# Kernel optimization log

Measured on AMD Instinct MI355X. Metric: run time of the kernel, lower is better.

The kernel has to match this reference:

```python
import jax, jax.numpy as jnp
import numpy as np

D1, D2, DK, NH = 1024, 1024, 1024, 1
B, S = 4, 2048


def setup_inputs() -> dict:
    key = jax.random.key(0)
    ks = jax.random.split(key, 12)
    scale1 = 1.0 / np.sqrt(D1)
    scale2 = 1.0 / np.sqrt(D2)
    scalek = 1.0 / np.sqrt(DK)
    return {
        "x": jax.random.normal(ks[0], (B, S, D1), dtype=jnp.float32),
        "y": jax.random.normal(ks[1], (B, S, D2), dtype=jnp.float32),
        "adj": jax.random.uniform(ks[2], (B, S, S), dtype=jnp.float32),
        "Wq": jax.random.uniform(ks[3], (D1, DK), jnp.float32, -scale1, scale1),
        "bq": jax.random.uniform(ks[4], (DK,), jnp.float32, -scale1, scale1),
        "Wk": jax.random.uniform(ks[5], (D2, DK), jnp.float32, -scale2, scale2),
        "bk": jax.random.uniform(ks[6], (DK,), jnp.float32, -scale2, scale2),
        "Wv": jax.random.uniform(ks[7], (D2, DK), jnp.float32, -scale2, scale2),
        "bv": jax.random.uniform(ks[8], (DK,), jnp.float32, -scale2, scale2),
        "Wo": jax.random.uniform(ks[9], (DK, D2), jnp.float32, -scalek, scalek),
        "bo": jax.random.uniform(ks[10], (D2,), jnp.float32, -scalek, scalek),
    }


def reference(x, y, adj, Wq, bq, Wk, bk, Wv, bv, Wo, bo):
    # Single-head (n_heads=1) cross-attention with additive adjacency bias.
    dk_head = DK // NH
    norm = 1.0 / np.sqrt(DK)
    Q = (x @ Wq + bq).reshape(NH, B, S, dk_head)   # [h,b,s,d]
    K = (y @ Wk + bk).reshape(NH, B, S, dk_head)
    V = (y @ Wv + bv).reshape(NH, B, S, dk_head)
    att = jnp.einsum('hbsd,hbtd->hbst', Q, K) * norm  # [h,b,s,t]
    att = jax.nn.softmax(att + adj, axis=-1)          # adj [b,s,t] broadcasts over h
    tmp = jnp.einsum('hbst,hbtd->hbsd', att, V).reshape(B, S, -1)  # [b,s,dk]
    out = (tmp @ Wo + bo).reshape(-1, S, D2)
    return out
```

## Files before the change

### kernel.cpp

```cpp
#include <hip/hip_runtime.h>
#include <stdint.h>

typedef unsigned short u16;
using bf16x8 = __attribute__((ext_vector_type(8))) short;
using f32x4  = __attribute__((ext_vector_type(4))) float;

#define NORM 0.03125f

enum { M_BF16_BIAS = 0, M_BF16T_BIAS = 1, M_EXP = 2, M_PV = 3, M_F32_BIAS = 4 };

__device__ __forceinline__ u16 f2bf(float f) {
  uint32_t u = __float_as_uint(f);
  return (u16)((u + 0x7FFFu + ((u >> 16) & 1u)) >> 16);
}

__device__ __forceinline__ void gload_lds16(const void* g, void* lds) {
  __builtin_amdgcn_global_load_lds(
      (const __attribute__((address_space(1))) uint32_t*)g,
      (__attribute__((address_space(3))) uint32_t*)lds, 16, 0, 0);
}

__global__ void k_cvt(const float* __restrict__ in, u16* __restrict__ out, int n4) {
  int i = blockIdx.x * blockDim.x + threadIdx.x;
  if (i >= n4) return;
  float4 v = ((const float4*)in)[i];
  uint32_t lo = f2bf(v.x) | ((uint32_t)f2bf(v.y) << 16);
  uint32_t hi = f2bf(v.z) | ((uint32_t)f2bf(v.w) << 16);
  ((uint2*)out)[i] = make_uint2(lo, hi);
}

__global__ void k_tc(const float* __restrict__ W0, const float* __restrict__ W1,
                     const float* __restrict__ W2, const float* __restrict__ W3,
                     u16* __restrict__ dst) {
  __shared__ float t[64][65];
  const float* W = blockIdx.z == 0 ? W0 : blockIdx.z == 1 ? W1 : blockIdx.z == 2 ? W2 : W3;
  u16* WT = dst + (size_t)blockIdx.z * (1024 * 1024);
  int c0 = blockIdx.x * 64, r0 = blockIdx.y * 64;
  int c = threadIdx.x & 63, q = threadIdx.x >> 6;
  for (int r = q; r < 64; r += 4) t[r][c] = W[(size_t)(r0 + r) * 1024 + c0 + c];
  __syncthreads();
  for (int r = q; r < 64; r += 4) WT[(size_t)(c0 + r) * 1024 + r0 + c] = f2bf(t[c][r]);
}

template <int MODE>
__global__ __launch_bounds__(256, 2) void gemm_bt(
    const u16* __restrict__ A, int lda, const u16* __restrict__ Bsrc, int ldb,
    long long bstrideB, int K, const float* __restrict__ bias,
    const float* __restrict__ adj, float* __restrict__ dpart,
    const float* __restrict__ dpart_r, void* __restrict__ Cout, int ldc) {
  __shared__ u16 As[128 * 64];
  __shared__ u16 Bs[128 * 64];

  const int tid = threadIdx.x;
  const int lane = tid & 63;
  const int wid = tid >> 6;
  const int wr = wid >> 1, wc = wid & 1;

  const int m0 = blockIdx.x * 128;
  const int n0 = blockIdx.y * 128;
  const int b = m0 >> 11;
  const u16* Bp = Bsrc + (size_t)b * bstrideB;

  f32x4 acc[4][4] = {};

  const int ric = lane >> 3;
  const int col8 = (lane & 7) * 8;

  for (int kt = 0; kt < K; kt += 64) {
#pragma unroll
    for (int c = 0; c < 4; ++c) {
      int ch = wid * 4 + c;
      int row = ch * 8 + ric;
      gload_lds16(A + (size_t)(m0 + row) * lda + kt + col8, (void*)&As[ch * 512]);
      gload_lds16(Bp + (size_t)(n0 + row) * ldb + kt + col8, (void*)&Bs[ch * 512]);
    }
    __syncthreads();
#pragma unroll
    for (int kk = 0; kk < 64; kk += 32) {
      bf16x8 af[4], bfr[4];
#pragma unroll
      for (int m = 0; m < 4; ++m)
        af[m] = *(const bf16x8*)&As[(wr * 64 + m * 16 + (lane & 15)) * 64 + kk + (lane >> 4) * 8];
#pragma unroll
      for (int n = 0; n < 4; ++n)
        bfr[n] = *(const bf16x8*)&Bs[(wc * 64 + n * 16 + (lane & 15)) * 64 + kk + (lane >> 4) * 8];
#pragma unroll
      for (int m = 0; m < 4; ++m)
#pragma unroll
        for (int n = 0; n < 4; ++n)
          acc[m][n] = __builtin_amdgcn_mfma_f32_16x16x32_bf16(af[m], bfr[n], acc[m][n], 0, 0, 0);
    }
    __syncthreads();
  }

  const int lr = lane >> 4;
  const int lc = lane & 15;

  if constexpr (MODE == M_BF16_BIAS) {
    u16* C = (u16*)Cout;
#pragma unroll
    for (int m = 0; m < 4; ++m)
#pragma unroll
      for (int n = 0; n < 4; ++n) {
        int gcol = n0 + wc * 64 + n * 16 + lc;
        float bvv = bias[gcol];
#pragma unroll
        for (int r = 0; r < 4; ++r) {
          int grow = m0 + wr * 64 + m * 16 + lr * 4 + r;
          C[(size_t)grow * ldc + gcol] = f2bf(acc[m][n][r] + bvv);
        }
      }
  } else if constexpr (MODE == M_BF16T_BIAS) {
    u16* C = (u16*)Cout;
#pragma unroll
    for (int m = 0; m < 4; ++m)
#pragma unroll
      for (int n = 0; n < 4; ++n) {
        int gcol = n0 + wc * 64 + n * 16 + lc;
        float bvv = bias[gcol];
        int grow0 = m0 + wr * 64 + m * 16 + lr * 4;
        int t0 = grow0 & 2047;
        ushort4 pk = make_ushort4(f2bf(acc[m][n][0] + bvv), f2bf(acc[m][n][1] + bvv),
                                  f2bf(acc[m][n][2] + bvv), f2bf(acc[m][n][3] + bvv));
        *(ushort4*)&C[((size_t)b * 1024 + gcol) * 2048 + t0] = pk;
      }
  } else if constexpr (MODE == M_EXP) {
    u16* C = (u16*)Cout;
    float esum[4][4] = {};
#pragma unroll
    for (int m = 0; m < 4; ++m)
#pragma unroll
      for (int n = 0; n < 4; ++n) {
        int gcol = n0 + wc * 64 + n * 16 + lc;
#pragma unroll
        for (int r = 0; r < 4; ++r) {
          int grow = m0 + wr * 64 + m * 16 + lr * 4 + r;
          float z = acc[m][n][r] * NORM + adj[(size_t)grow * 2048 + gcol];
          float e = __expf(z);
          C[(size_t)grow * 2048 + gcol] = f2bf(e);
          esum[m][r] += e;
        }
      }
    int pidx = blockIdx.y * 2 + wc;
#pragma unroll
    for (int m = 0; m < 4; ++m)
#pragma unroll
      for (int r = 0; r < 4; ++r) {
        float s = esum[m][r];
        s += __shfl_xor(s, 1);
        s += __shfl_xor(s, 2);
        s += __shfl_xor(s, 4);
        s += __shfl_xor(s, 8);
        if (lc == 0)
          dpart[(size_t)pidx * 8192 + (m0 + wr * 64 + m * 16 + lr * 4 + r)] = s;
      }
  } else if constexpr (MODE == M_PV) {
    __shared__ float dinv[128];
    if (tid < 128) {
      float s = 0.f;
      for (int t = 0; t < 32; ++t) s += dpart_r[(size_t)t * 8192 + m0 + tid];
      dinv[tid] = 1.0f / s;
    }
    __syncthreads();
    u16* C = (u16*)Cout;
#pragma unroll
    for (int m = 0; m < 4; ++m)
#pragma unroll
      for (int n = 0; n < 4; ++n) {
        int gcol = n0 + wc * 64 + n * 16 + lc;
#pragma unroll
        for (int r = 0; r < 4; ++r) {
          int lrow = wr * 64 + m * 16 + lr * 4 + r;
          C[(size_t)(m0 + lrow) * ldc + gcol] = f2bf(acc[m][n][r] * dinv[lrow]);
        }
      }
  } else {
    float* C = (float*)Cout;
#pragma unroll
    for (int m = 0; m < 4; ++m)
#pragma unroll
      for (int n = 0; n < 4; ++n) {
        int gcol = n0 + wc * 64 + n * 16 + lc;
        float bvv = bias[gcol];
#pragma unroll
        for (int r = 0; r < 4; ++r) {
          int grow = m0 + wr * 64 + m * 16 + lr * 4 + r;
          C[(size_t)grow * ldc + gcol] = acc[m][n][r] + bvv;
        }
      }
  }
}

extern "C" void kernel_launch(void* const* d_in, const int* in_sizes, int n_in,
                              void* d_out, int out_size, void* d_ws, size_t ws_size,
                              hipStream_t stream) {
  const float* x   = (const float*)d_in[0];
  const float* y   = (const float*)d_in[1];
  const float* adj = (const float*)d_in[2];
  const float* Wq  = (const float*)d_in[3];
  const float* bq  = (const float*)d_in[4];
  const float* Wk  = (const float*)d_in[5];
  const float* bk  = (const float*)d_in[6];
  const float* Wv  = (const float*)d_in[7];
  const float* bv  = (const float*)d_in[8];
  const float* Wo  = (const float*)d_in[9];
  const float* bo  = (const float*)d_in[10];
  float* out = (float*)d_out;

  char* ws = (char*)d_ws;
  if (ws_size < 143654912ULL) return;
  u16* xb = (u16*)(ws);
  u16* yb = (u16*)(ws + 16777216);
  u16* WT = (u16*)(ws + 33554432);
  u16* Qb = (u16*)(ws + 41943040);
  u16* Kb = (u16*)(ws + 58720256);
  u16* Vt = (u16*)(ws + 75497472);
  u16* E  = (u16*)(ws + 92274688);
  float* dpart = (float*)(ws + 125829120);
  u16* tmpb = (u16*)(ws + 126877696);

  u16* WqT = WT;
  u16* WkT = WT + 1048576;
  u16* WvT = WT + 2097152;
  u16* WoT = WT + 3145728;

  k_cvt<<<8192, 256, 0, stream>>>(x, xb, 2097152);
  k_cvt<<<8192, 256, 0, stream>>>(y, yb, 2097152);
  k_tc<<<dim3(16, 16, 4), 256, 0, stream>>>(Wq, Wk, Wv, Wo, WT);

  gemm_bt<M_BF16_BIAS><<<dim3(64, 8), 256, 0, stream>>>(
      xb, 1024, WqT, 1024, 0, 1024, bq, nullptr, nullptr, nullptr, Qb, 1024);
  gemm_bt<M_BF16_BIAS><<<dim3(64, 8), 256, 0, stream>>>(
      yb, 1024, WkT, 1024, 0, 1024, bk, nullptr, nullptr, nullptr, Kb, 1024);
  gemm_bt<M_BF16T_BIAS><<<dim3(64, 8), 256, 0, stream>>>(
      yb, 1024, WvT, 1024, 0, 1024, bv, nullptr, nullptr, nullptr, Vt, 2048);

  gemm_bt<M_EXP><<<dim3(64, 16), 256, 0, stream>>>(
      Qb, 1024, Kb, 1024, 2097152LL, 1024, nullptr, adj, dpart, nullptr, E, 2048);

  gemm_bt<M_PV><<<dim3(64, 8), 256, 0, stream>>>(
      E, 2048, Vt, 2048, 2097152LL, 2048, nullptr, nullptr, nullptr, dpart, tmpb, 1024);

  gemm_bt<M_F32_BIAS><<<dim3(64, 8), 256, 0, stream>>>(
      tmpb, 1024, WoT, 1024, 0, 1024, bo, nullptr, nullptr, nullptr, out, 1024);
}
```

Measured before the change: 271.5 us.

## Replace GEMMs with 256x256 double-buffered swizzled kernel and merge QKV launches

Replaces the 128x128, 4-wave GEMM with a 256x256-tile, 8-wave kernel. It double-buffers a 128 KB LDS stage, uses XOR-swizzled LDS layouts, and issues the next K-slices' async global-to-LDS loads between MFMA phases, with explicit vmcnt/lgkmcnt waits and s_setprio. The Q, K and V projections are merged into one launch indexed by blockIdx.z. The goal is more data reuse per tile and hiding load latency behind MFMA. In exchange, grids shrink, so the PV and output GEMMs launch only 128 blocks, and the large LDS footprint limits occupancy to one block per CU.

```diff
diff --git a/kernel.cpp b/kernel.cpp
--- a/kernel.cpp
+++ b/kernel.cpp
@@ -7,7 +7,7 @@
 
 #define NORM 0.03125f
 
-enum { M_BF16_BIAS = 0, M_BF16T_BIAS = 1, M_EXP = 2, M_PV = 3, M_F32_BIAS = 4 };
+enum { M_PROJ = 0, M_EXP = 1, M_PV = 2, M_OUT = 3 };
 
 __device__ __forceinline__ u16 f2bf(float f) {
   uint32_t u = __float_as_uint(f);
@@ -42,152 +42,223 @@
   for (int r = q; r < 64; r += 4) WT[(size_t)(c0 + r) * 1024 + r0 + c] = f2bf(t[c][r]);
 }
 
+struct GArgs {
+  const u16* A; const u16* B; int lda, ldb; long long bstrideB; int K;
+  const float* bias; const float* adj; float* dpart; const float* dpart_r;
+  void* C; int ldc;
+  const u16* A1; const u16* B1; const u16* B2;
+  const float* bias1; const float* bias2; void* C1; void* C2;
+};
+
 template <int MODE>
-__global__ __launch_bounds__(256, 2) void gemm_bt(
-    const u16* __restrict__ A, int lda, const u16* __restrict__ Bsrc, int ldb,
-    long long bstrideB, int K, const float* __restrict__ bias,
-    const float* __restrict__ adj, float* __restrict__ dpart,
-    const float* __restrict__ dpart_r, void* __restrict__ Cout, int ldc) {
-  __shared__ u16 As[128 * 64];
-  __shared__ u16 Bs[128 * 64];
-
-  const int tid = threadIdx.x;
-  const int lane = tid & 63;
-  const int wid = tid >> 6;
-  const int wr = wid >> 1, wc = wid & 1;
-
-  const int m0 = blockIdx.x * 128;
-  const int n0 = blockIdx.y * 128;
+__global__ __launch_bounds__(512, 2) void gemm8(GArgs g) {
+  __shared__ __align__(16) u16 sm[65536];
+
+  const int tid = threadIdx.x, lane = tid & 63, wid = tid >> 6;
+  const int wm = wid >> 2, wn = wid & 3;
+  const int m0 = blockIdx.x * 256;
+  const int n0 = blockIdx.y * 256;
   const int b = m0 >> 11;
-  const u16* Bp = Bsrc + (size_t)b * bstrideB;
-
-  f32x4 acc[4][4] = {};
-
-  const int ric = lane >> 3;
-  const int col8 = (lane & 7) * 8;
-
-  for (int kt = 0; kt < K; kt += 64) {
-#pragma unroll
-    for (int c = 0; c < 4; ++c) {
-      int ch = wid * 4 + c;
-      int row = ch * 8 + ric;
-      gload_lds16(A + (size_t)(m0 + row) * lda + kt + col8, (void*)&As[ch * 512]);
-      gload_lds16(Bp + (size_t)(n0 + row) * ldb + kt + col8, (void*)&Bs[ch * 512]);
+
+  const u16* A = g.A; const u16* B = g.B;
+  const float* bias = g.bias; void* C = g.C;
+  int zmode = 0;
+  if constexpr (MODE == M_PROJ) {
+    int z = blockIdx.z; zmode = z;
+    if (z == 1) { A = g.A1; B = g.B1; bias = g.bias1; C = g.C1; }
+    else if (z == 2) { A = g.A1; B = g.B2; bias = g.bias2; C = g.C2; }
+  }
+  const int lda = g.lda, ldb = g.ldb, K = g.K, NT = K >> 6;
+  const u16* Bp = B + (size_t)b * g.bstrideB;
+
+  f32x4 acc[8][4] = {};
+
+  auto stage = [&](const u16* src, int ld, int r0, int kc, int dst_u16) {
+#pragma unroll
+    for (int j = 0; j < 2; ++j) {
+      int row = wid * 16 + j * 128 + (lane >> 2);
+      int cb = (lane & 3) * 16;
+      int csw = cb ^ ((row & 8) << 2);
+      gload_lds16(src + (size_t)(r0 + row) * ld + kc + (csw >> 1),
+                  (void*)&sm[dst_u16 + wid * 512 + j * 4096]);
+    }
+  };
+  auto stA = [&](int v, int kh) {
+    stage(A, lda, m0, v * 64 + kh * 32, (v & 1) * 32768 + kh * 8192);
+  };
+  auto stB = [&](int v, int kh) {
+    stage(Bp, ldb, n0, v * 64 + kh * 32, (v & 1) * 32768 + 16384 + kh * 8192);
+  };
+
+  stA(0, 0); stB(0, 0); stA(0, 1); stB(0, 1);
+  stA(1, 0); stB(1, 0);
+  __builtin_amdgcn_sched_barrier(0);
+  asm volatile("s_waitcnt vmcnt(8)" ::: "memory");
+  __builtin_amdgcn_sched_barrier(0);
+  __builtin_amdgcn_s_barrier();
+  __builtin_amdgcn_sched_barrier(0);
+
+  const int cb = (lane >> 4) * 16;
+  for (int u = 0; u < NT; ++u) {
+    const int base = (u & 1) * 32768;
+#pragma unroll
+    for (int ph = 0; ph < 4; ++ph) {
+      const int h = ph & 1, kh = ph >> 1;
+      bf16x8 af[4], bfr[4];
+#pragma unroll
+      for (int m = 0; m < 4; ++m) {
+        int row = wm * 128 + h * 64 + m * 16 + (lane & 15);
+        af[m] = *(const bf16x8*)__builtin_assume_aligned(
+            &sm[base + kh * 8192 + row * 32 + ((cb ^ ((row & 8) << 2)) >> 1)], 16);
+      }
+#pragma unroll
+      for (int n = 0; n < 4; ++n) {
+        int row = wn * 64 + n * 16 + (lane & 15);
+        bfr[n] = *(const bf16x8*)__builtin_assume_aligned(
+            &sm[base + 16384 + kh * 8192 + row * 32 + ((cb ^ ((row & 8) << 2)) >> 1)], 16);
+      }
+      if (ph == 0) {
+        if (u + 1 < NT) stA(u + 1, 1);
+      } else if (ph == 1) {
+        if (u + 1 < NT) stB(u + 1, 1);
+        __builtin_amdgcn_sched_barrier(0);
+        if (u + 1 < NT) asm volatile("s_waitcnt vmcnt(4)" ::: "memory");
+        else            asm volatile("s_waitcnt vmcnt(0)" ::: "memory");
+        __builtin_amdgcn_sched_barrier(0);
+      } else if (ph == 2) {
+        if (u + 2 < NT) stA(u + 2, 0);
+      } else {
+        if (u + 2 < NT) stB(u + 2, 0);
+      }
+      __builtin_amdgcn_s_barrier();
+      __builtin_amdgcn_sched_barrier(0);
+      __builtin_amdgcn_s_setprio(1);
+#pragma unroll
+      for (int m = 0; m < 4; ++m)
+#pragma unroll
+        for (int n = 0; n < 4; ++n)
+          acc[h * 4 + m][n] = __builtin_amdgcn_mfma_f32_16x16x32_bf16(
+              af[m], bfr[n], acc[h * 4 + m][n], 0, 0, 0);
+      __builtin_amdgcn_s_setprio(0);
+      __builtin_amdgcn_sched_barrier(0);
+      asm volatile("s_waitcnt lgkmcnt(0)" ::: "memory");
+      __builtin_amdgcn_sched_barrier(0);
+      __builtin_amdgcn_s_barrier();
+      __builtin_amdgcn_sched_barrier(0);
+    }
+  }
+
+  const int lr = lane >> 4, lc = lane & 15;
+
+  if constexpr (MODE == M_PROJ) {
+    if (zmode < 2) {
+      u16* Cc = (u16*)C;
+#pragma unroll
+      for (int i = 0; i < 8; ++i) {
+        int rowo = (i >> 2) * 64 + (i & 3) * 16;
+#pragma unroll
+        for (int n = 0; n < 4; ++n) {
+          int gcol = n0 + wn * 64 + n * 16 + lc;
+          float bv = bias[gcol];
+#pragma unroll
+          for (int r = 0; r < 4; ++r) {
+            int grow = m0 + wm * 128 + rowo + lr * 4 + r;
+            Cc[(size_t)grow * g.ldc + gcol] = f2bf(acc[i][n][r] + bv);
+          }
+        }
+      }
+    } else {
+      u16* Cc = (u16*)C;
+#pragma unroll
+      for (int i = 0; i < 8; ++i) {
+        int rowo = (i >> 2) * 64 + (i & 3) * 16;
+        int grow0 = m0 + wm * 128 + rowo + lr * 4;
+        int t0 = grow0 & 2047;
+#pragma unroll
+        for (int n = 0; n < 4; ++n) {
+          int gcol = n0 + wn * 64 + n * 16 + lc;
+          float bv = bias[gcol];
+          ushort4 pk = make_ushort4(f2bf(acc[i][n][0] + bv), f2bf(acc[i][n][1] + bv),
+                                    f2bf(acc[i][n][2] + bv), f2bf(acc[i][n][3] + bv));
+          *(ushort4*)&Cc[((size_t)b * 1024 + gcol) * 2048 + t0] = pk;
+        }
+      }
+    }
+  } else if constexpr (MODE == M_EXP) {
+    u16* Cc = (u16*)C;
+    float esum[8][4];
+#pragma unroll
+    for (int i = 0; i < 8; ++i)
+#pragma unroll
+      for (int r = 0; r < 4; ++r) esum[i][r] = 0.f;
+#pragma unroll
+    for (int i = 0; i < 8; ++i) {
+      int rowo = (i >> 2) * 64 + (i & 3) * 16;
+#pragma unroll
+      for (int n = 0; n < 4; ++n) {
+        int gcol = n0 + wn * 64 + n * 16 + lc;
+#pragma unroll
+        for (int r = 0; r < 4; ++r) {
+          int grow = m0 + wm * 128 + rowo + lr * 4 + r;
+          float z = acc[i][n][r] * NORM + g.adj[(size_t)grow * 2048 + gcol];
+          float e = __expf(z);
+          Cc[(size_t)grow * 2048 + gcol] = f2bf(e);
+          esum[i][r] += e;
+        }
+      }
+    }
+    int pidx = blockIdx.y * 4 + wn;
+#pragma unroll
+    for (int i = 0; i < 8; ++i) {
+      int rowo = (i >> 2) * 64 + (i & 3) * 16;
+#pragma unroll
+      for (int r = 0; r < 4; ++r) {
+        float s = esum[i][r];
+        s += __shfl_xor(s, 1); s += __shfl_xor(s, 2);
+        s += __shfl_xor(s, 4); s += __shfl_xor(s, 8);
+        if (lc == 0)
+          g.dpart[(size_t)pidx * 8192 + m0 + wm * 128 + rowo + lr * 4 + r] = s;
+      }
+    }
+  } else if constexpr (MODE == M_PV) {
+    __shared__ float dinv[256];
+    if (tid < 256) {
+      float s = 0.f;
+#pragma unroll
+      for (int t = 0; t < 32; ++t) s += g.dpart_r[(size_t)t * 8192 + m0 + tid];
+      dinv[tid] = 1.0f / s;
     }
     __syncthreads();
-#pragma unroll
-    for (int kk = 0; kk < 64; kk += 32) {
-      bf16x8 af[4], bfr[4];
-#pragma unroll
-      for (int m = 0; m < 4; ++m)
-        af[m] = *(const bf16x8*)&As[(wr * 64 + m * 16 + (lane & 15)) * 64 + kk + (lane >> 4) * 8];
-#pragma unroll
-      for (int n = 0; n < 4; ++n)
-        bfr[n] = *(const bf16x8*)&Bs[(wc * 64 + n * 16 + (lane & 15)) * 64 + kk + (lane >> 4) * 8];
-#pragma unroll
-      for (int m = 0; m < 4; ++m)
-#pragma unroll
-        for (int n = 0; n < 4; ++n)
-          acc[m][n] = __builtin_amdgcn_mfma_f32_16x16x32_bf16(af[m], bfr[n], acc[m][n], 0, 0, 0);
-    }
-    __syncthreads();
-  }
-
-  const int lr = lane >> 4;
-  const int lc = lane & 15;
-
-  if constexpr (MODE == M_BF16_BIAS) {
-    u16* C = (u16*)Cout;
-#pragma unroll
-    for (int m = 0; m < 4; ++m)
+    u16* Cc = (u16*)C;
+#pragma unroll
+    for (int i = 0; i < 8; ++i) {
+      int rowo = (i >> 2) * 64 + (i & 3) * 16;
 #pragma unroll
       for (int n = 0; n < 4; ++n) {
-        int gcol = n0 + wc * 64 + n * 16 + lc;
-        float bvv = bias[gcol];
+        int gcol = n0 + wn * 64 + n * 16 + lc;
 #pragma unroll
         for (int r = 0; r < 4; ++r) {
-          int grow = m0 + wr * 64 + m * 16 + lr * 4 + r;
-          C[(size_t)grow * ldc + gcol] = f2bf(acc[m][n][r] + bvv);
-        }
-      }
-  } else if constexpr (MODE == M_BF16T_BIAS) {
-    u16* C = (u16*)Cout;
-#pragma unroll
-    for (int m = 0; m < 4; ++m)
+          int lrow = wm * 128 + rowo + lr * 4 + r;
+          Cc[(size_t)(m0 + lrow) * g.ldc + gcol] = f2bf(acc[i][n][r] * dinv[lrow]);
+        }
+      }
+    }
+  } else {
+    float* Cc = (float*)C;
+#pragma unroll
+    for (int i = 0; i < 8; ++i) {
+      int rowo = (i >> 2) * 64 + (i & 3) * 16;
 #pragma unroll
       for (int n = 0; n < 4; ++n) {
-        int gcol = n0 + wc * 64 + n * 16 + lc;
-        float bvv = bias[gcol];
-        int grow0 = m0 + wr * 64 + m * 16 + lr * 4;
-        int t0 = grow0 & 2047;
-        ushort4 pk = make_ushort4(f2bf(acc[m][n][0] + bvv), f2bf(acc[m][n][1] + bvv),
-                                  f2bf(acc[m][n][2] + bvv), f2bf(acc[m][n][3] + bvv));
-        *(ushort4*)&C[((size_t)b * 1024 + gcol) * 2048 + t0] = pk;
-      }
-  } else if constexpr (MODE == M_EXP) {
-    u16* C = (u16*)Cout;
-    float esum[4][4] = {};
-#pragma unroll
-    for (int m = 0; m < 4; ++m)
-#pragma unroll
-      for (int n = 0; n < 4; ++n) {
-        int gcol = n0 + wc * 64 + n * 16 + lc;
+        int gcol = n0 + wn * 64 + n * 16 + lc;
+        float bv = bias[gcol];
 #pragma unroll
         for (int r = 0; r < 4; ++r) {
-          int grow = m0 + wr * 64 + m * 16 + lr * 4 + r;
-          float z = acc[m][n][r] * NORM + adj[(size_t)grow * 2048 + gcol];
-          float e = __expf(z);
-          C[(size_t)grow * 2048 + gcol] = f2bf(e);
-          esum[m][r] += e;
-        }
-      }
-    int pidx = blockIdx.y * 2 + wc;
-#pragma unroll
-    for (int m = 0; m < 4; ++m)
-#pragma unroll
-      for (int r = 0; r < 4; ++r) {
-        float s = esum[m][r];
-        s += __shfl_xor(s, 1);
-        s += __shfl_xor(s, 2);
-        s += __shfl_xor(s, 4);
-        s += __shfl_xor(s, 8);
-        if (lc == 0)
-          dpart[(size_t)pidx * 8192 + (m0 + wr * 64 + m * 16 + lr * 4 + r)] = s;
-      }
-  } else if constexpr (MODE == M_PV) {
-    __shared__ float dinv[128];
-    if (tid < 128) {
-      float s = 0.f;
-      for (int t = 0; t < 32; ++t) s += dpart_r[(size_t)t * 8192 + m0 + tid];
-      dinv[tid] = 1.0f / s;
-    }
-    __syncthreads();
-    u16* C = (u16*)Cout;
-#pragma unroll
-    for (int m = 0; m < 4; ++m)
-#pragma unroll
-      for (int n = 0; n < 4; ++n) {
-        int gcol = n0 + wc * 64 + n * 16 + lc;
-#pragma unroll
-        for (int r = 0; r < 4; ++r) {
-          int lrow = wr * 64 + m * 16 + lr * 4 + r;
-          C[(size_t)(m0 + lrow) * ldc + gcol] = f2bf(acc[m][n][r] * dinv[lrow]);
-        }
-      }
-  } else {
-    float* C = (float*)Cout;
-#pragma unroll
-    for (int m = 0; m < 4; ++m)
-#pragma unroll
-      for (int n = 0; n < 4; ++n) {
-        int gcol = n0 + wc * 64 + n * 16 + lc;
-        float bvv = bias[gcol];
-#pragma unroll
-        for (int r = 0; r < 4; ++r) {
-          int grow = m0 + wr * 64 + m * 16 + lr * 4 + r;
-          C[(size_t)grow * ldc + gcol] = acc[m][n][r] + bvv;
-        }
-      }
+          int grow = m0 + wm * 128 + rowo + lr * 4 + r;
+          Cc[(size_t)grow * g.ldc + gcol] = acc[i][n][r] + bv;
+        }
+      }
+    }
   }
 }
 
@@ -228,19 +299,29 @@
   k_cvt<<<8192, 256, 0, stream>>>(y, yb, 2097152);
   k_tc<<<dim3(16, 16, 4), 256, 0, stream>>>(Wq, Wk, Wv, Wo, WT);
 
-  gemm_bt<M_BF16_BIAS><<<dim3(64, 8), 256, 0, stream>>>(
-      xb, 1024, WqT, 1024, 0, 1024, bq, nullptr, nullptr, nullptr, Qb, 1024);
-  gemm_bt<M_BF16_BIAS><<<dim3(64, 8), 256, 0, stream>>>(
-      yb, 1024, WkT, 1024, 0, 1024, bk, nullptr, nullptr, nullptr, Kb, 1024);
-  gemm_bt<M_BF16T_BIAS><<<dim3(64, 8), 256, 0, stream>>>(
-      yb, 1024, WvT, 1024, 0, 1024, bv, nullptr, nullptr, nullptr, Vt, 2048);
-
-  gemm_bt<M_EXP><<<dim3(64, 16), 256, 0, stream>>>(
-      Qb, 1024, Kb, 1024, 2097152LL, 1024, nullptr, adj, dpart, nullptr, E, 2048);
-
-  gemm_bt<M_PV><<<dim3(64, 8), 256, 0, stream>>>(
-      E, 2048, Vt, 2048, 2097152LL, 2048, nullptr, nullptr, nullptr, dpart, tmpb, 1024);
-
-  gemm_bt<M_F32_BIAS><<<dim3(64, 8), 256, 0, stream>>>(
-      tmpb, 1024, WoT, 1024, 0, 1024, bo, nullptr, nullptr, nullptr, out, 1024);
-}
+  GArgs ga;
+  ga.A = xb; ga.B = WqT; ga.lda = 1024; ga.ldb = 1024; ga.bstrideB = 0; ga.K = 1024;
+  ga.bias = bq; ga.adj = nullptr; ga.dpart = nullptr; ga.dpart_r = nullptr;
+  ga.C = Qb; ga.ldc = 1024;
+  ga.A1 = yb; ga.B1 = WkT; ga.B2 = WvT; ga.bias1 = bk; ga.bias2 = bv;
+  ga.C1 = Kb; ga.C2 = Vt;
+  gemm8<M_PROJ><<<dim3(32, 4, 3), 512, 0, stream>>>(ga);
+
+  GArgs ge = {};
+  ge.A = Qb; ge.B = Kb; ge.lda = 1024; ge.ldb = 1024; ge.bstrideB = 2097152LL; ge.K = 1024;
+  ge.bias = nullptr; ge.adj = adj; ge.dpart = dpart; ge.dpart_r = nullptr;
+  ge.C = E; ge.ldc = 2048;
+  gemm8<M_EXP><<<dim3(32, 8), 512, 0, stream>>>(ge);
+
+  GArgs gp = {};
+  gp.A = E; gp.B = Vt; gp.lda = 2048; gp.ldb = 2048; gp.bstrideB = 2097152LL; gp.K = 2048;
+  gp.bias = nullptr; gp.adj = nullptr; gp.dpart = nullptr; gp.dpart_r = dpart;
+  gp.C = tmpb; gp.ldc = 1024;
+  gemm8<M_PV><<<dim3(32, 4), 512, 0, stream>>>(gp);
+
+  GArgs go = {};
+  go.A = tmpb; go.B = WoT; go.lda = 1024; go.ldb = 1024; go.bstrideB = 0; go.K = 1024;
+  go.bias = bo; go.adj = nullptr; go.dpart = nullptr; go.dpart_r = nullptr;
+  go.C = out; go.ldc = 1024;
+  gemm8<M_OUT><<<dim3(32, 4), 512, 0, stream>>>(go);
+}
```

New measurement: 266.7 us. No clear change (-1.8%).
